# Performance work log

Measured on AMD Instinct MI355X. Metric: run time of the kernel, lower is better.

Reference implementation:

```python
import jax, jax.numpy as jnp
import numpy as np

R_SAFE = 0.8

def setup_inputs() -> dict:
    key = jax.random.key(0)
    ks = jax.random.split(key, 12)
    B, F, H1, H21, H22, C = 524288, 10, 128, 32, 32, 2
    def lin(k, fan_in, fan_out):
        k1, k2 = jax.random.split(k)
        bound = 1.0 / np.sqrt(fan_in)
        W = jax.random.uniform(k1, (fan_out, fan_in), jnp.float32, -bound, bound)
        b = jax.random.uniform(k2, (fan_out,), jnp.float32, -bound, bound)
        return W, b
    W1, b1 = lin(ks[0], F, H1)
    W21, b21 = lin(ks[1], H1, H21)
    W22, b22 = lin(ks[2], H1, H22)
    W31, b31 = lin(ks[3], H21, C)
    W32, b32 = lin(ks[4], H22, 1)
    obs = jax.random.normal(ks[5], (B, F), jnp.float32)
    return {"obs": obs, "W1": W1, "b1": b1, "W21": W21, "b21": b21,
            "W22": W22, "b22": b22, "W31": W31, "b31": b31, "W32": W32, "b32": b32}

def _forward(obs, W1, b1, W21, b21, W22, b22, W31, b31, W32, b32):
    x = jax.nn.silu(obs @ W1.T + b1)          # [B, H1]
    x21 = jax.nn.silu(x @ W21.T + b21)        # [B, H21]
    x22 = jax.nn.silu(x @ W22.T + b22)        # [B, H22]
    unom = x21 @ W31.T + b31                  # [B, 2]
    alpha = 4.0 * jax.nn.sigmoid((x22 @ W32.T + b32)[:, 0])  # [B]
    rel_x, rel_y = obs[:, 6], obs[:, 7]
    v_hx, v_hy = obs[:, 8], obs[:, 9]
    barrier = rel_x**2 + rel_y**2 - R_SAFE**2
    lf = -2.0 * (rel_x * v_hx + rel_y * v_hy)
    # single inequality G u <= h with G = [-2 rel_x, -2 rel_y]
    G = jnp.stack([-2.0 * rel_x, -2.0 * rel_y], axis=1)      # [B, 2]
    h = lf + alpha * barrier                                  # [B]
    # QP: min ||u - unom||^2 s.t. G u <= h  ->  halfspace projection (exact KKT)
    gg = jnp.sum(G * G, axis=1)                               # [B]
    viol = jnp.sum(G * unom, axis=1) - h                      # [B]
    lam = jnp.where(gg > 0, jax.nn.relu(viol) / jnp.maximum(gg, 1e-12), 0.0)
    return unom - lam[:, None] * G

def reference(obs, W1, b1, W21, b21, W22, b22, W31, b31, W32, b32):
    return _forward(obs, W1, b1, W21, b21, W22, b22, W31, b31, W32, b32)
```

## Files before the change

kernel.cpp:

```cpp
#include <hip/hip_runtime.h>


typedef _Float16 half8 __attribute__((ext_vector_type(8)));
typedef float floatx4 __attribute__((ext_vector_type(4)));

#define TPB   256
#define NW    4
#define GRID  4096
#define XSTR  136

#define WS_FRAG 0
#define WS_B1   26624
#define WS_B2   28672
#define WS_B3   29696

__device__ __forceinline__ float fast_sigmoid(float z) {
    return __builtin_amdgcn_rcpf(1.0f + __expf(-z));
}

__global__ __launch_bounds__(256) void prep_kernel(
    const float* __restrict__ W1,  const float* __restrict__ b1,
    const float* __restrict__ W21, const float* __restrict__ b21,
    const float* __restrict__ W22, const float* __restrict__ b22,
    const float* __restrict__ W31, const float* __restrict__ b31,
    const float* __restrict__ W32, const float* __restrict__ b32,
    unsigned char* __restrict__ ws)
{
    const int tid  = blockIdx.x * 256 + threadIdx.x;
    const int lane = tid & 63;
    const int m    = lane & 15;
    const int q    = lane >> 4;

    if (tid < 26 * 64) {
        const int f = tid >> 6;
        float v[8];
        if (f < 8) {
            const float* wr = W1 + (f * 16 + m) * 10;
            #pragma unroll
            for (int j = 0; j < 8; ++j) {
                const int k = q * 8 + j;
                v[j] = (k < 10) ? wr[k] : 0.0f;
            }
        } else if (f < 24) {
            const int f2 = f - 8, nt2 = f2 >> 2, kt = f2 & 3;
            const int n2 = nt2 * 16 + m;
            const float* wr = (n2 < 32) ? (W21 + n2 * 128)
                                        : (W22 + (n2 - 32) * 128);
            #pragma unroll
            for (int j = 0; j < 8; ++j) v[j] = wr[kt * 32 + q * 8 + j];
        } else if (f == 24) {
            #pragma unroll
            for (int j = 0; j < 8; ++j)
                v[j] = (m < 2) ? W31[m * 32 + q * 8 + j] : 0.0f;
        } else {
            #pragma unroll
            for (int j = 0; j < 8; ++j)
                v[j] = (m == 2) ? W32[q * 8 + j] : 0.0f;
        }
        half8 h;
        #pragma unroll
        for (int j = 0; j < 8; ++j) h[j] = (_Float16)v[j];
        ((half8*)(ws + WS_FRAG))[tid] = h;
    }
    if (tid < 512)
        ((float*)(ws + WS_B1))[tid] = b1[(tid >> 6) * 16 + (tid & 15)];
    if (tid < 256) {
        const int n2 = (tid >> 6) * 16 + (tid & 15);
        ((float*)(ws + WS_B2))[tid] = (n2 < 32) ? b21[n2] : b22[n2 - 32];
    }
    if (tid < 64) {
        const int mm = tid & 15;
        ((float*)(ws + WS_B3))[tid] =
            (mm == 0) ? b31[0] : (mm == 1) ? b31[1] : (mm == 2) ? b32[0] : 0.0f;
    }
}

__global__ __launch_bounds__(TPB, 2) void barriernet_kernel(
    const float* __restrict__ obs,
    const unsigned char* __restrict__ ws,
    float* __restrict__ out, int B)
{
    __shared__ _Float16 xs[NW * 2 * 16 * XSTR];
    __shared__ float    ep[NW * 2 * 16 * 4];

    const int tid  = threadIdx.x;
    const int wave = tid >> 6;
    const int lane = tid & 63;
    const int m    = lane & 15;
    const int q    = lane >> 4;

    const half8* wf = (const half8*)(ws + WS_FRAG);
    half8 w1f[8], w2f[16], w3f0, w3f1;
    #pragma unroll
    for (int nt = 0; nt < 8; ++nt)  w1f[nt] = wf[nt * 64 + lane];
    #pragma unroll
    for (int f2 = 0; f2 < 16; ++f2) w2f[f2] = wf[(8 + f2) * 64 + lane];
    w3f0 = wf[24 * 64 + lane];
    w3f1 = wf[25 * 64 + lane];

    const float* fB1 = (const float*)(ws + WS_B1);
    const float* fB2 = (const float*)(ws + WS_B2);
    float b1f[8], b2f[4];
    #pragma unroll
    for (int nt = 0; nt < 8; ++nt) b1f[nt] = fB1[nt * 64 + lane];
    #pragma unroll
    for (int nt2 = 0; nt2 < 4; ++nt2) b2f[nt2] = fB2[nt2 * 64 + lane];
    const float b3v = ((const float*)(ws + WS_B3))[lane];

    const int tiles = (B + 15) >> 4;
    const int tbase = (blockIdx.x * NW + wave) * 2;

    _Float16*    xq[2];
    const half8* xr[2];
    float*       epw[2];
    #pragma unroll
    for (int p = 0; p < 2; ++p) {
        _Float16* xw = xs + (wave * 2 + p) * 16 * XSTR;
        xq[p]  = xw + q * 4 * XSTR + m;
        xr[p]  = (const half8*)(xw + m * XSTR + q * 8);
        epw[p] = ep + (wave * 2 + p) * 16 * 4;
    }

    const float* orow[2];
    half8 a1[2];
    int lrow0[2];
    #pragma unroll
    for (int p = 0; p < 2; ++p) {
        int tile = tbase + p;
        if (tile >= tiles) tile = tiles - 1;
        int lr = (tile << 4) + m;
        if (lr >= B) lr = B - 1;
        lrow0[p] = lr;
        orow[p] = obs + (size_t)lr * 10;

        float g0=0,g1=0,g2=0,g3=0,g4=0,g5=0,g6=0,g7=0;
        if (q == 0) {
            float2 p0 = *(const float2*)(orow[p] + 0);
            float2 p1 = *(const float2*)(orow[p] + 2);
            float2 p2 = *(const float2*)(orow[p] + 4);
            float2 p3 = *(const float2*)(orow[p] + 6);
            g0=p0.x; g1=p0.y; g2=p1.x; g3=p1.y;
            g4=p2.x; g5=p2.y; g6=p3.x; g7=p3.y;
        } else if (q == 1) {
            float2 pp = *(const float2*)(orow[p] + 8);
            g0=pp.x; g1=pp.y;
        }
        a1[p][0]=(_Float16)g0; a1[p][1]=(_Float16)g1;
        a1[p][2]=(_Float16)g2; a1[p][3]=(_Float16)g3;
        a1[p][4]=(_Float16)g4; a1[p][5]=(_Float16)g5;
        a1[p][6]=(_Float16)g6; a1[p][7]=(_Float16)g7;
    }

    #pragma unroll
    for (int nt = 0; nt < 8; ++nt) {
        #pragma unroll
        for (int p = 0; p < 2; ++p) {
            floatx4 z = {b1f[nt], b1f[nt], b1f[nt], b1f[nt]};
            z = __builtin_amdgcn_mfma_f32_16x16x32_f16(a1[p], w1f[nt], z, 0, 0, 0);
            #pragma unroll
            for (int r = 0; r < 4; ++r) {
                float zz = z[r];
                xq[p][r * XSTR + nt * 16] = (_Float16)(zz * fast_sigmoid(zz));
            }
        }
    }

    half8 a2[2][4];
    #pragma unroll
    for (int p = 0; p < 2; ++p)
        #pragma unroll
        for (int kt = 0; kt < 4; ++kt) a2[p][kt] = xr[p][kt * 4];

    #pragma unroll
    for (int nt2 = 0; nt2 < 4; ++nt2) {
        #pragma unroll
        for (int p = 0; p < 2; ++p) {
            floatx4 z = {b2f[nt2], b2f[nt2], b2f[nt2], b2f[nt2]};
            #pragma unroll
            for (int kt = 0; kt < 4; ++kt)
                z = __builtin_amdgcn_mfma_f32_16x16x32_f16(a2[p][kt], w2f[nt2 * 4 + kt], z, 0, 0, 0);
            #pragma unroll
            for (int r = 0; r < 4; ++r) {
                float zz = z[r];
                xq[p][r * XSTR + nt2 * 16] = (_Float16)(zz * fast_sigmoid(zz));
            }
        }
    }

    #pragma unroll
    for (int p = 0; p < 2; ++p) {
        half8 a30 = xr[p][0];
        half8 a31 = xr[p][4];
        floatx4 d = {b3v, b3v, b3v, b3v};
        d = __builtin_amdgcn_mfma_f32_16x16x32_f16(a30, w3f0, d, 0, 0, 0);
        d = __builtin_amdgcn_mfma_f32_16x16x32_f16(a31, w3f1, d, 0, 0, 0);
        if (m < 3) {
            #pragma unroll
            for (int r = 0; r < 4; ++r)
                epw[p][(q * 4 + r) * 4 + m] = d[r];
        }
    }

    #pragma unroll
    for (int p = 0; p < 2; ++p) {
        if (q == 0) {
            float4 e = ((const float4*)epw[p])[m];
            const float u0 = e.x, u1 = e.y, z32 = e.z;
            const float alpha = 4.0f * fast_sigmoid(z32);

            const float2 rxy = *(const float2*)(orow[p] + 6);
            const float2 vxy = *(const float2*)(orow[p] + 8);
            const float rx = rxy.x, ry = rxy.y, vx = vxy.x, vy = vxy.y;

            const float barrier = rx * rx + ry * ry - 0.64f;
            const float lf = -2.0f * (rx * vx + ry * vy);
            const float gx = -2.0f * rx, gy = -2.0f * ry;
            const float h  = lf + alpha * barrier;
            const float gg = gx * gx + gy * gy;
            const float viol = gx * u0 + gy * u1 - h;
            float lam = 0.0f;
            if (gg > 0.0f) lam = fmaxf(viol, 0.0f) / fmaxf(gg, 1e-12f);

            float2 r;
            r.x = fmaf(-lam, gx, u0);
            r.y = fmaf(-lam, gy, u1);
            *(float2*)(out + (size_t)lrow0[p] * 2) = r;
        }
    }
}

extern "C" void kernel_launch(void* const* d_in, const int* in_sizes, int n_in,
                              void* d_out, int out_size, void* d_ws, size_t ws_size,
                              hipStream_t stream) {
    const float* obs = (const float*)d_in[0];
    const float* W1  = (const float*)d_in[1];
    const float* b1  = (const float*)d_in[2];
    const float* W21 = (const float*)d_in[3];
    const float* b21 = (const float*)d_in[4];
    const float* W22 = (const float*)d_in[5];
    const float* b22 = (const float*)d_in[6];
    const float* W31 = (const float*)d_in[7];
    const float* b31 = (const float*)d_in[8];
    const float* W32 = (const float*)d_in[9];
    const float* b32 = (const float*)d_in[10];

    unsigned char* ws = (unsigned char*)d_ws;

    prep_kernel<<<7, 256, 0, stream>>>(W1, b1, W21, b21, W22, b22,
                                       W31, b31, W32, b32, ws);

    const int B = in_sizes[0] / 10;
    const int tiles = (B + 15) / 16;
    const int pairs = (tiles + 1) / 2;
    const int grid  = (pairs + NW - 1) / NW;

    barriernet_kernel<<<grid, TPB, 0, stream>>>(obs, ws, (float*)d_out, B);
}
```

Baseline: 120.1 us.

## Stage weight fragments in LDS and reuse one activation buffer per wave

The kernel no longer holds all 26 half8 weight fragments in registers. The whole workspace is copied into shared memory once per block and fragments are read from LDS on demand. The two row tiles per wave are now processed one after another through a single shared activation buffer, which halves the xs footprint. Launch bounds rise from 2 to 3 blocks per CU to use the lower register pressure, at the cost of an extra block-wide LDS fill, a barrier and more LDS reads per MFMA.

```diff
diff --git a/kernel.cpp b/kernel.cpp
--- a/kernel.cpp
+++ b/kernel.cpp
@@ -6,13 +6,17 @@
 
 #define TPB   256
 #define NW    4
-#define GRID  4096
 #define XSTR  136
 
 #define WS_FRAG 0
 #define WS_B1   26624
 #define WS_B2   28672
 #define WS_B3   29696
+#define WS_END  29952
+
+#define L_XS    29952
+#define L_EP    (29952 + NW*16*XSTR*2)
+#define L_TOTAL (L_EP + NW*2*16*4*4)
 
 __device__ __forceinline__ float fast_sigmoid(float z) {
     return __builtin_amdgcn_rcpf(1.0f + __expf(-z));
@@ -75,13 +79,12 @@
     }
 }
 
-__global__ __launch_bounds__(TPB, 2) void barriernet_kernel(
+__global__ __launch_bounds__(TPB, 3) void barriernet_kernel(
     const float* __restrict__ obs,
     const unsigned char* __restrict__ ws,
     float* __restrict__ out, int B)
 {
-    __shared__ _Float16 xs[NW * 2 * 16 * XSTR];
-    __shared__ float    ep[NW * 2 * 16 * 4];
+    __shared__ __align__(16) unsigned char lds[L_TOTAL];
 
     const int tid  = threadIdx.x;
     const int wave = tid >> 6;
@@ -89,37 +92,35 @@
     const int m    = lane & 15;
     const int q    = lane >> 4;
 
-    const half8* wf = (const half8*)(ws + WS_FRAG);
-    half8 w1f[8], w2f[16], w3f0, w3f1;
-    #pragma unroll
-    for (int nt = 0; nt < 8; ++nt)  w1f[nt] = wf[nt * 64 + lane];
-    #pragma unroll
-    for (int f2 = 0; f2 < 16; ++f2) w2f[f2] = wf[(8 + f2) * 64 + lane];
-    w3f0 = wf[24 * 64 + lane];
-    w3f1 = wf[25 * 64 + lane];
-
-    const float* fB1 = (const float*)(ws + WS_B1);
-    const float* fB2 = (const float*)(ws + WS_B2);
+    {
+        const float4* src = (const float4*)ws;
+        float4* dst = (float4*)lds;
+        for (int i = tid; i < WS_END / 16; i += TPB) dst[i] = src[i];
+    }
+    __syncthreads();
+
+    const _Float16* wl  = (const _Float16*)lds;
+    const float*    lb1 = (const float*)(lds + WS_B1);
+    const float*    lb2 = (const float*)(lds + WS_B2);
+    const float*    lb3 = (const float*)(lds + WS_B3);
+
     float b1f[8], b2f[4];
     #pragma unroll
-    for (int nt = 0; nt < 8; ++nt) b1f[nt] = fB1[nt * 64 + lane];
-    #pragma unroll
-    for (int nt2 = 0; nt2 < 4; ++nt2) b2f[nt2] = fB2[nt2 * 64 + lane];
-    const float b3v = ((const float*)(ws + WS_B3))[lane];
+    for (int nt = 0; nt < 8; ++nt) b1f[nt] = lb1[nt * 64 + lane];
+    #pragma unroll
+    for (int nt2 = 0; nt2 < 4; ++nt2) b2f[nt2] = lb2[nt2 * 64 + lane];
+    const float b3v = lb3[lane];
+
+    const _Float16* wbase = wl + lane * 8;
+    #define WFRAG(f) (*(const half8*)(wbase + (f) * 512))
+
+    _Float16* xsl = (_Float16*)(lds + L_XS) + wave * 16 * XSTR;
+    _Float16* xq  = xsl + q * 4 * XSTR + m;
+    const half8* xr = (const half8*)(xsl + m * XSTR + q * 8);
+    float* epw = (float*)(lds + L_EP) + wave * 2 * 64;
 
     const int tiles = (B + 15) >> 4;
     const int tbase = (blockIdx.x * NW + wave) * 2;
-
-    _Float16*    xq[2];
-    const half8* xr[2];
-    float*       epw[2];
-    #pragma unroll
-    for (int p = 0; p < 2; ++p) {
-        _Float16* xw = xs + (wave * 2 + p) * 16 * XSTR;
-        xq[p]  = xw + q * 4 * XSTR + m;
-        xr[p]  = (const half8*)(xw + m * XSTR + q * 8);
-        epw[p] = ep + (wave * 2 + p) * 16 * 4;
-    }
 
     const float* orow[2];
     half8 a1[2];
@@ -151,60 +152,81 @@
         a1[p][6]=(_Float16)g6; a1[p][7]=(_Float16)g7;
     }
 
+    half8 a2[2][4];
+
     #pragma unroll
     for (int nt = 0; nt < 8; ++nt) {
-        #pragma unroll
-        for (int p = 0; p < 2; ++p) {
-            floatx4 z = {b1f[nt], b1f[nt], b1f[nt], b1f[nt]};
-            z = __builtin_amdgcn_mfma_f32_16x16x32_f16(a1[p], w1f[nt], z, 0, 0, 0);
-            #pragma unroll
-            for (int r = 0; r < 4; ++r) {
-                float zz = z[r];
-                xq[p][r * XSTR + nt * 16] = (_Float16)(zz * fast_sigmoid(zz));
-            }
-        }
-    }
-
-    half8 a2[2][4];
-    #pragma unroll
-    for (int p = 0; p < 2; ++p)
-        #pragma unroll
-        for (int kt = 0; kt < 4; ++kt) a2[p][kt] = xr[p][kt * 4];
-
+        floatx4 z = {b1f[nt], b1f[nt], b1f[nt], b1f[nt]};
+        z = __builtin_amdgcn_mfma_f32_16x16x32_f16(a1[0], WFRAG(nt), z, 0, 0, 0);
+        #pragma unroll
+        for (int r = 0; r < 4; ++r) {
+            float zz = z[r];
+            xq[r * XSTR + nt * 16] = (_Float16)(zz * fast_sigmoid(zz));
+        }
+    }
+    #pragma unroll
+    for (int kt = 0; kt < 4; ++kt) a2[0][kt] = xr[kt * 4];
+
+    #pragma unroll
+    for (int nt = 0; nt < 8; ++nt) {
+        floatx4 z = {b1f[nt], b1f[nt], b1f[nt], b1f[nt]};
+        z = __builtin_amdgcn_mfma_f32_16x16x32_f16(a1[1], WFRAG(nt), z, 0, 0, 0);
+        #pragma unroll
+        for (int r = 0; r < 4; ++r) {
+            float zz = z[r];
+            xq[r * XSTR + nt * 16] = (_Float16)(zz * fast_sigmoid(zz));
+        }
+    }
+    #pragma unroll
+    for (int kt = 0; kt < 4; ++kt) a2[1][kt] = xr[kt * 4];
+
+    half8 a3[2][2];
     #pragma unroll
     for (int nt2 = 0; nt2 < 4; ++nt2) {
-        #pragma unroll
-        for (int p = 0; p < 2; ++p) {
-            floatx4 z = {b2f[nt2], b2f[nt2], b2f[nt2], b2f[nt2]};
-            #pragma unroll
-            for (int kt = 0; kt < 4; ++kt)
-                z = __builtin_amdgcn_mfma_f32_16x16x32_f16(a2[p][kt], w2f[nt2 * 4 + kt], z, 0, 0, 0);
-            #pragma unroll
-            for (int r = 0; r < 4; ++r) {
-                float zz = z[r];
-                xq[p][r * XSTR + nt2 * 16] = (_Float16)(zz * fast_sigmoid(zz));
-            }
-        }
-    }
+        floatx4 z = {b2f[nt2], b2f[nt2], b2f[nt2], b2f[nt2]};
+        #pragma unroll
+        for (int kt = 0; kt < 4; ++kt)
+            z = __builtin_amdgcn_mfma_f32_16x16x32_f16(a2[0][kt], WFRAG(8 + nt2 * 4 + kt), z, 0, 0, 0);
+        #pragma unroll
+        for (int r = 0; r < 4; ++r) {
+            float zz = z[r];
+            xq[r * XSTR + nt2 * 16] = (_Float16)(zz * fast_sigmoid(zz));
+        }
+    }
+    a3[0][0] = xr[0];
+    a3[0][1] = xr[4];
+
+    #pragma unroll
+    for (int nt2 = 0; nt2 < 4; ++nt2) {
+        floatx4 z = {b2f[nt2], b2f[nt2], b2f[nt2], b2f[nt2]};
+        #pragma unroll
+        for (int kt = 0; kt < 4; ++kt)
+            z = __builtin_amdgcn_mfma_f32_16x16x32_f16(a2[1][kt], WFRAG(8 + nt2 * 4 + kt), z, 0, 0, 0);
+        #pragma unroll
+        for (int r = 0; r < 4; ++r) {
+            float zz = z[r];
+            xq[r * XSTR + nt2 * 16] = (_Float16)(zz * fast_sigmoid(zz));
+        }
+    }
+    a3[1][0] = xr[0];
+    a3[1][1] = xr[4];
 
     #pragma unroll
     for (int p = 0; p < 2; ++p) {
-        half8 a30 = xr[p][0];
-        half8 a31 = xr[p][4];
         floatx4 d = {b3v, b3v, b3v, b3v};
-        d = __builtin_amdgcn_mfma_f32_16x16x32_f16(a30, w3f0, d, 0, 0, 0);
-        d = __builtin_amdgcn_mfma_f32_16x16x32_f16(a31, w3f1, d, 0, 0, 0);
+        d = __builtin_amdgcn_mfma_f32_16x16x32_f16(a3[p][0], WFRAG(24), d, 0, 0, 0);
+        d = __builtin_amdgcn_mfma_f32_16x16x32_f16(a3[p][1], WFRAG(25), d, 0, 0, 0);
         if (m < 3) {
             #pragma unroll
             for (int r = 0; r < 4; ++r)
-                epw[p][(q * 4 + r) * 4 + m] = d[r];
+                epw[p * 64 + (q * 4 + r) * 4 + m] = d[r];
         }
     }
 
     #pragma unroll
     for (int p = 0; p < 2; ++p) {
         if (q == 0) {
-            float4 e = ((const float4*)epw[p])[m];
+            float4 e = ((const float4*)(epw + p * 64))[m];
             const float u0 = e.x, u1 = e.y, z32 = e.z;
             const float alpha = 4.0f * fast_sigmoid(z32);
 
@@ -227,6 +249,7 @@
             *(float2*)(out + (size_t)lrow0[p] * 2) = r;
         }
     }
+    #undef WFRAG
 }
 
 extern "C" void kernel_launch(void* const* d_in, const int* in_sizes, int n_in,
```

Result: slower. 125.8 us (+4.7%).

## Keep MLP activations in registers via transposed MFMA chaining, drop LDS staging

Applied to the files above, without the earlier changes.

Swaps the MFMA operand order so each layer computes the transposed product. The accumulator layout of one layer then serves directly as the B-operand fragment of the next, so activations stay in registers and the shared-memory round trips and their buffers are removed. The layer-1 bias is folded into the weight fragment through a constant-1 input column, and the output biases are read directly. This lowers LDS traffic and shared-memory use per block, in exchange for a more intricate weight packing whose correctness depends on exact fragment index mapping.

```diff
diff --git a/kernel.cpp b/kernel.cpp
--- a/kernel.cpp
+++ b/kernel.cpp
@@ -4,15 +4,11 @@
 typedef _Float16 half8 __attribute__((ext_vector_type(8)));
 typedef float floatx4 __attribute__((ext_vector_type(4)));
 
-#define TPB   256
-#define NW    4
-#define GRID  4096
-#define XSTR  136
+#define TPB 256
+#define NW  4
 
 #define WS_FRAG 0
-#define WS_B1   26624
-#define WS_B2   28672
-#define WS_B3   29696
+#define WS_B2Q  26624
 
 __device__ __forceinline__ float fast_sigmoid(float z) {
     return __builtin_amdgcn_rcpf(1.0f + __expf(-z));
@@ -39,7 +35,7 @@
             #pragma unroll
             for (int j = 0; j < 8; ++j) {
                 const int k = q * 8 + j;
-                v[j] = (k < 10) ? wr[k] : 0.0f;
+                v[j] = (k < 10) ? wr[k] : (k == 10 ? b1[f * 16 + m] : 0.0f);
             }
         } else if (f < 24) {
             const int f2 = f - 8, nt2 = f2 >> 2, kt = f2 & 3;
@@ -47,42 +43,46 @@
             const float* wr = (n2 < 32) ? (W21 + n2 * 128)
                                         : (W22 + (n2 - 32) * 128);
             #pragma unroll
-            for (int j = 0; j < 8; ++j) v[j] = wr[kt * 32 + q * 8 + j];
-        } else if (f == 24) {
-            #pragma unroll
-            for (int j = 0; j < 8; ++j)
-                v[j] = (m < 2) ? W31[m * 32 + q * 8 + j] : 0.0f;
+            for (int j = 0; j < 8; ++j) {
+                const int H = (2 * kt + (j >> 2)) * 16 + q * 4 + (j & 3);
+                v[j] = wr[H];
+            }
         } else {
-            #pragma unroll
-            for (int j = 0; j < 8; ++j)
-                v[j] = (m == 2) ? W32[q * 8 + j] : 0.0f;
+            const int kt3 = f - 24;
+            #pragma unroll
+            for (int j = 0; j < 8; ++j) {
+                const int H3 = (2 * kt3 + (j >> 2)) * 16 + q * 4 + (j & 3);
+                float x = 0.0f;
+                if (m == 0)      x = (H3 < 32)  ? W31[H3]       : 0.0f;
+                else if (m == 1) x = (H3 < 32)  ? W31[32 + H3]  : 0.0f;
+                else if (m == 2) x = (H3 >= 32) ? W32[H3 - 32]  : 0.0f;
+                v[j] = x;
+            }
         }
         half8 h;
         #pragma unroll
         for (int j = 0; j < 8; ++j) h[j] = (_Float16)v[j];
         ((half8*)(ws + WS_FRAG))[tid] = h;
     }
-    if (tid < 512)
-        ((float*)(ws + WS_B1))[tid] = b1[(tid >> 6) * 16 + (tid & 15)];
-    if (tid < 256) {
-        const int n2 = (tid >> 6) * 16 + (tid & 15);
-        ((float*)(ws + WS_B2))[tid] = (n2 < 32) ? b21[n2] : b22[n2 - 32];
-    }
-    if (tid < 64) {
-        const int mm = tid & 15;
-        ((float*)(ws + WS_B3))[tid] =
-            (mm == 0) ? b31[0] : (mm == 1) ? b31[1] : (mm == 2) ? b32[0] : 0.0f;
+    if (tid < 16) {
+        const int nt2 = tid >> 2, qq = tid & 3;
+        float4 v;
+        float* vp = (float*)&v;
+        #pragma unroll
+        for (int r = 0; r < 4; ++r) {
+            const int n2 = nt2 * 16 + qq * 4 + r;
+            vp[r] = (n2 < 32) ? b21[n2] : b22[n2 - 32];
+        }
+        ((float4*)(ws + WS_B2Q))[tid] = v;
     }
 }
 
 __global__ __launch_bounds__(TPB, 2) void barriernet_kernel(
     const float* __restrict__ obs,
     const unsigned char* __restrict__ ws,
+    const float* __restrict__ b31, const float* __restrict__ b32,
     float* __restrict__ out, int B)
 {
-    __shared__ _Float16 xs[NW * 2 * 16 * XSTR];
-    __shared__ float    ep[NW * 2 * 16 * 4];
-
     const int tid  = threadIdx.x;
     const int wave = tid >> 6;
     const int lane = tid & 63;
@@ -98,31 +98,18 @@
     w3f0 = wf[24 * 64 + lane];
     w3f1 = wf[25 * 64 + lane];
 
-    const float* fB1 = (const float*)(ws + WS_B1);
-    const float* fB2 = (const float*)(ws + WS_B2);
-    float b1f[8], b2f[4];
-    #pragma unroll
-    for (int nt = 0; nt < 8; ++nt) b1f[nt] = fB1[nt * 64 + lane];
-    #pragma unroll
-    for (int nt2 = 0; nt2 < 4; ++nt2) b2f[nt2] = fB2[nt2 * 64 + lane];
-    const float b3v = ((const float*)(ws + WS_B3))[lane];
+    const float4* bt = (const float4*)(ws + WS_B2Q);
+    float4 b2q[4];
+    #pragma unroll
+    for (int nt2 = 0; nt2 < 4; ++nt2) b2q[nt2] = bt[nt2 * 4 + q];
+
+    const float bu0 = b31[0], bu1 = b31[1], bz3 = b32[0];
 
     const int tiles = (B + 15) >> 4;
     const int tbase = (blockIdx.x * NW + wave) * 2;
 
-    _Float16*    xq[2];
-    const half8* xr[2];
-    float*       epw[2];
-    #pragma unroll
-    for (int p = 0; p < 2; ++p) {
-        _Float16* xw = xs + (wave * 2 + p) * 16 * XSTR;
-        xq[p]  = xw + q * 4 * XSTR + m;
-        xr[p]  = (const half8*)(xw + m * XSTR + q * 8);
-        epw[p] = ep + (wave * 2 + p) * 16 * 4;
-    }
-
     const float* orow[2];
-    half8 a1[2];
+    half8 xf[2];
     int lrow0[2];
     #pragma unroll
     for (int p = 0; p < 2; ++p) {
@@ -144,68 +131,82 @@
         } else if (q == 1) {
             float2 pp = *(const float2*)(orow[p] + 8);
             g0=pp.x; g1=pp.y;
-        }
-        a1[p][0]=(_Float16)g0; a1[p][1]=(_Float16)g1;
-        a1[p][2]=(_Float16)g2; a1[p][3]=(_Float16)g3;
-        a1[p][4]=(_Float16)g4; a1[p][5]=(_Float16)g5;
-        a1[p][6]=(_Float16)g6; a1[p][7]=(_Float16)g7;
-    }
-
+            g2=1.0f;
+        }
+        xf[p][0]=(_Float16)g0; xf[p][1]=(_Float16)g1;
+        xf[p][2]=(_Float16)g2; xf[p][3]=(_Float16)g3;
+        xf[p][4]=(_Float16)g4; xf[p][5]=(_Float16)g5;
+        xf[p][6]=(_Float16)g6; xf[p][7]=(_Float16)g7;
+    }
+
+    floatx4 acc[2][8];
     #pragma unroll
     for (int nt = 0; nt < 8; ++nt) {
         #pragma unroll
         for (int p = 0; p < 2; ++p) {
-            floatx4 z = {b1f[nt], b1f[nt], b1f[nt], b1f[nt]};
-            z = __builtin_amdgcn_mfma_f32_16x16x32_f16(a1[p], w1f[nt], z, 0, 0, 0);
-            #pragma unroll
-            for (int r = 0; r < 4; ++r) {
-                float zz = z[r];
-                xq[p][r * XSTR + nt * 16] = (_Float16)(zz * fast_sigmoid(zz));
-            }
-        }
-    }
-
-    half8 a2[2][4];
-    #pragma unroll
-    for (int p = 0; p < 2; ++p)
-        #pragma unroll
-        for (int kt = 0; kt < 4; ++kt) a2[p][kt] = xr[p][kt * 4];
-
+            floatx4 z = {0.0f, 0.0f, 0.0f, 0.0f};
+            acc[p][nt] = __builtin_amdgcn_mfma_f32_16x16x32_f16(
+                             w1f[nt], xf[p], z, 0, 0, 0);
+        }
+    }
+
+    half8 b2f[2][4];
+    #pragma unroll
+    for (int p = 0; p < 2; ++p) {
+        #pragma unroll
+        for (int kt = 0; kt < 4; ++kt) {
+            half8 bf;
+            #pragma unroll
+            for (int jj = 0; jj < 4; ++jj) {
+                float z0 = acc[p][2 * kt][jj];
+                float z1 = acc[p][2 * kt + 1][jj];
+                bf[jj]     = (_Float16)(z0 * fast_sigmoid(z0));
+                bf[jj + 4] = (_Float16)(z1 * fast_sigmoid(z1));
+            }
+            b2f[p][kt] = bf;
+        }
+    }
+
+    floatx4 acc2[2][4];
     #pragma unroll
     for (int nt2 = 0; nt2 < 4; ++nt2) {
         #pragma unroll
         for (int p = 0; p < 2; ++p) {
-            floatx4 z = {b2f[nt2], b2f[nt2], b2f[nt2], b2f[nt2]};
+            floatx4 z = {b2q[nt2].x, b2q[nt2].y, b2q[nt2].z, b2q[nt2].w};
             #pragma unroll
             for (int kt = 0; kt < 4; ++kt)
-                z = __builtin_amdgcn_mfma_f32_16x16x32_f16(a2[p][kt], w2f[nt2 * 4 + kt], z, 0, 0, 0);
-            #pragma unroll
-            for (int r = 0; r < 4; ++r) {
-                float zz = z[r];
-                xq[p][r * XSTR + nt2 * 16] = (_Float16)(zz * fast_sigmoid(zz));
-            }
-        }
-    }
-
-    #pragma unroll
-    for (int p = 0; p < 2; ++p) {
-        half8 a30 = xr[p][0];
-        half8 a31 = xr[p][4];
-        floatx4 d = {b3v, b3v, b3v, b3v};
-        d = __builtin_amdgcn_mfma_f32_16x16x32_f16(a30, w3f0, d, 0, 0, 0);
-        d = __builtin_amdgcn_mfma_f32_16x16x32_f16(a31, w3f1, d, 0, 0, 0);
-        if (m < 3) {
-            #pragma unroll
-            for (int r = 0; r < 4; ++r)
-                epw[p][(q * 4 + r) * 4 + m] = d[r];
-        }
-    }
-
-    #pragma unroll
-    for (int p = 0; p < 2; ++p) {
+                z = __builtin_amdgcn_mfma_f32_16x16x32_f16(
+                        w2f[nt2 * 4 + kt], b2f[p][kt], z, 0, 0, 0);
+            acc2[p][nt2] = z;
+        }
+    }
+
+    half8 b3f[2][2];
+    #pragma unroll
+    for (int p = 0; p < 2; ++p) {
+        #pragma unroll
+        for (int kt3 = 0; kt3 < 2; ++kt3) {
+            half8 bf;
+            #pragma unroll
+            for (int jj = 0; jj < 4; ++jj) {
+                float z0 = acc2[p][2 * kt3][jj];
+                float z1 = acc2[p][2 * kt3 + 1][jj];
+                bf[jj]     = (_Float16)(z0 * fast_sigmoid(z0));
+                bf[jj + 4] = (_Float16)(z1 * fast_sigmoid(z1));
+            }
+            b3f[p][kt3] = bf;
+        }
+    }
+
+    #pragma unroll
+    for (int p = 0; p < 2; ++p) {
+        floatx4 d = {0.0f, 0.0f, 0.0f, 0.0f};
+        d = __builtin_amdgcn_mfma_f32_16x16x32_f16(w3f0, b3f[p][0], d, 0, 0, 0);
+        d = __builtin_amdgcn_mfma_f32_16x16x32_f16(w3f1, b3f[p][1], d, 0, 0, 0);
         if (q == 0) {
-            float4 e = ((const float4*)epw[p])[m];
-            const float u0 = e.x, u1 = e.y, z32 = e.z;
+            const float u0  = d[0] + bu0;
+            const float u1  = d[1] + bu1;
+            const float z32 = d[2] + bz3;
             const float alpha = 4.0f * fast_sigmoid(z32);
 
             const float2 rxy = *(const float2*)(orow[p] + 6);
@@ -254,5 +255,6 @@
     const int pairs = (tiles + 1) / 2;
     const int grid  = (pairs + NW - 1) / NW;
 
-    barriernet_kernel<<<grid, TPB, 0, stream>>>(obs, ws, (float*)d_out, B);
-}
+    barriernet_kernel<<<grid, TPB, 0, stream>>>(obs, ws, b31, b32,
+                                                (float*)d_out, B);
+}
```

After: 124.0 us. 1.03x slower.
